# Performance work log

Measured on AMD Instinct MI355X. Metric: run time of the kernel, lower is better.

The kernel has to match this reference:

```python
import jax, jax.numpy as jnp
import numpy as np

NEG = -10000000000.0  # matches the torch module's additive mask value


def _span_attn(enc, logit_tok, starts, ends, qb, bsz):
    # enc: [bsz, seq, d]; logit_tok: [bsz, seq]; starts/ends/qb: [Q]
    seq = enc.shape[1]
    pos = jnp.arange(seq)
    # span mask: token t belongs to span iff start <= t <= end (inclusive)
    mask = (pos[None, :] >= starts[:, None]) & (pos[None, :] <= ends[:, None])  # [Q, seq]
    logits = logit_tok[qb] + (1.0 - mask.astype(enc.dtype)) * NEG               # [Q, seq]
    w = jax.nn.softmax(logits, axis=1)                                           # [Q, seq]
    # avoid materializing enc[qb] ([Q, seq, d]): contract against every batch row,
    # then select the right batch with a one-hot (p is tiny: [Q, bsz, d]).
    p = jnp.einsum('qs,bsd->qbd', w, enc)
    oh = jax.nn.one_hot(qb, bsz, dtype=enc.dtype)
    return jnp.einsum('qbd,qb->qd', p, oh)


def setup_inputs() -> dict:
    key = jax.random.key(0)
    ks = jax.random.split(key, 10)
    bsz, seq, hd, pd, Q = 8, 2048, 1024, 256, 8192
    enc = jax.random.normal(ks[0], (bsz, seq, hd), dtype=jnp.float32)
    proj_w = jax.random.normal(ks[1], (hd, pd), dtype=jnp.float32) * (1.0 / np.sqrt(hd))
    proj_b = jnp.zeros((pd,), dtype=jnp.float32)
    attn_w = jax.random.normal(ks[2], (pd,), dtype=jnp.float32) * (1.0 / np.sqrt(pd))
    attn_b = jnp.zeros((), dtype=jnp.float32)

    def make_spans(k):
        k1, k2, k3 = jax.random.split(k, 3)
        s = jax.random.randint(k1, (Q,), 0, seq)
        ln = jax.random.randint(k2, (Q,), 0, 32)
        e = jnp.minimum(s + ln, seq - 1)
        return s, e

    s1, e1 = make_spans(ks[3])
    s2, e2 = make_spans(ks[4])
    qb = jax.random.randint(ks[5], (Q,), 0, bsz)
    return {
        'flag': 0,
        'encoded_input': enc,
        'start_ids_1': s1,
        'end_ids_1': e1,
        'query_batch_idx': qb,
        'start_ids_2': s2,
        'end_ids_2': e2,
        'proj_w': proj_w,
        'proj_b': proj_b,
        'attn_w': attn_w,
        'attn_b': attn_b,
    }


def reference(flag, encoded_input, start_ids_1, end_ids_1, query_batch_idx,
              start_ids_2, end_ids_2, proj_w, proj_b, attn_w, attn_b):
    del flag  # unused in the original forward
    bsz = encoded_input.shape[0]
    enc = encoded_input @ proj_w + proj_b                 # use_proj=True path
    logit_tok = jnp.einsum('bsd,d->bs', enc, attn_w) + attn_b  # Linear(d,1)
    res1 = _span_attn(enc, logit_tok, start_ids_1, end_ids_1, query_batch_idx, bsz)
    res2 = _span_attn(enc, logit_tok, start_ids_2, end_ids_2, query_batch_idx, bsz)
    return (res1, res2)
```

## Files before the change

kernel.cpp:

```cpp
#include <hip/hip_runtime.h>

typedef __attribute__((ext_vector_type(8))) short bf16x8;
typedef __attribute__((ext_vector_type(4))) float f32x4;

#define LDK 40

__device__ __forceinline__ float bf2f(unsigned short u) {
    union { unsigned int i; float f; } v; v.i = ((unsigned int)u) << 16; return v.f;
}
__device__ __forceinline__ unsigned short f2bf(float f) {
    union { float f; unsigned int i; } v; v.f = f;
    unsigned int x = v.i;
    return (unsigned short)((x + 0x7FFFu + ((x >> 16) & 1u)) >> 16);
}

__global__ __launch_bounds__(256) void transpose_b_kernel(
    const float* __restrict__ B, unsigned short* __restrict__ Bt, int K, int N)
{
    __shared__ float tile[32][33];
    int kb = blockIdx.x % (K / 32);
    int nb = blockIdx.x / (K / 32);
    int k0 = kb * 32, n0 = nb * 32;
    int tx = threadIdx.x & 31, ty = threadIdx.x >> 5;
    #pragma unroll
    for (int i = 0; i < 4; ++i)
        tile[ty + 8 * i][tx] = B[(size_t)(k0 + ty + 8 * i) * N + n0 + tx];
    __syncthreads();
    #pragma unroll
    for (int i = 0; i < 4; ++i)
        Bt[(size_t)(n0 + ty + 8 * i) * K + k0 + tx] = f2bf(tile[tx][ty + 8 * i]);
}

__global__ __launch_bounds__(256, 4) void gemm_mfma_kernel(
    const float* __restrict__ A, const unsigned short* __restrict__ Bt,
    const float* __restrict__ bias, unsigned short* __restrict__ C,
    int M, int N, int K)
{
    __shared__ unsigned short Asl[2][64 * LDK];
    __shared__ unsigned short Bsl[2][64 * LDK];

    const int tid = threadIdx.x;
    const int bid = blockIdx.x;
    const int xcd = bid & 7;
    const int j   = bid >> 3;
    const int bn  = (j & 3) * 64;
    const int bm  = (xcd * 32 + (j >> 2)) * 64;

    const int lane = tid & 63;
    const int wave = tid >> 6;
    const int wr = (wave >> 1) * 32;
    const int wc = (wave & 1) * 32;

    const int srow = tid >> 2;
    const int sk   = (tid & 3) * 8;
    const float*          Aptr = A  + (size_t)(bm + srow) * K + sk;
    const unsigned short* Bptr = Bt + (size_t)(bn + srow) * K + sk;

    float4 areg[2];
    uint4  breg;

    f32x4 acc[2][2];
    #pragma unroll
    for (int m = 0; m < 2; ++m)
        #pragma unroll
        for (int n = 0; n < 2; ++n)
            acc[m][n] = (f32x4){0.f, 0.f, 0.f, 0.f};

    const int c15 = lane & 15;
    const int kg8 = (lane >> 4) * 8;

    #define LOAD_TILE(k0)                                                     \
        {                                                                     \
            areg[0] = *(const float4*)(Aptr + (k0));                          \
            areg[1] = *(const float4*)(Aptr + (k0) + 4);                      \
            breg    = *(const uint4*)(Bptr + (k0));                           \
        }

    #define STORE_TILE(buf)                                                   \
        {                                                                     \
            unsigned short tmp[8];                                            \
            const float* af = (const float*)areg;                             \
            _Pragma("unroll")                                                 \
            for (int i = 0; i < 8; ++i) tmp[i] = f2bf(af[i]);                 \
            *(bf16x8*)&Asl[buf][srow * LDK + sk] = *(bf16x8*)&tmp[0];         \
            *(uint4*)&Bsl[buf][srow * LDK + sk]  = breg;                      \
        }

    const int nk = K / 32;

    LOAD_TILE(0)
    STORE_TILE(0)
    __syncthreads();

    for (int t = 0; t < nk; ++t) {
        if (t + 1 < nk) LOAD_TILE((t + 1) * 32)

        const int buf = t & 1;
        bf16x8 af[2], bfr[2];
        #pragma unroll
        for (int m = 0; m < 2; ++m)
            af[m] = *(bf16x8*)&Asl[buf][(wr + m * 16 + c15) * LDK + kg8];
        #pragma unroll
        for (int n = 0; n < 2; ++n)
            bfr[n] = *(bf16x8*)&Bsl[buf][(wc + n * 16 + c15) * LDK + kg8];
        #pragma unroll
        for (int m = 0; m < 2; ++m)
            #pragma unroll
            for (int n = 0; n < 2; ++n)
                acc[m][n] = __builtin_amdgcn_mfma_f32_16x16x32_bf16(
                    af[m], bfr[n], acc[m][n], 0, 0, 0);

        if (t + 1 < nk) {
            STORE_TILE((t + 1) & 1)
            __syncthreads();
        }
    }

    const int col0 = bn + wc + c15;
    const int row0 = bm + wr + (lane >> 4) * 4;
    #pragma unroll
    for (int n = 0; n < 2; ++n) {
        float bv = bias[col0 + n * 16];
        #pragma unroll
        for (int m = 0; m < 2; ++m) {
            #pragma unroll
            for (int i = 0; i < 4; ++i) {
                C[(size_t)(row0 + m * 16 + i) * N + col0 + n * 16] =
                    f2bf(acc[m][n][i] + bv);
            }
        }
    }
    #undef LOAD_TILE
    #undef STORE_TILE
}

__global__ __launch_bounds__(256) void logit_kernel(
    const unsigned short* __restrict__ enc, const float* __restrict__ attn_w,
    float* __restrict__ logit, int rows)
{
    int gid = blockIdx.x * 256 + threadIdx.x;
    int row = gid >> 6, lane = gid & 63;
    if (row >= rows) return;
    ushort4 ev = *(const ushort4*)(enc + (size_t)row * 256 + lane * 4);
    float4  w  = ((const float4*)attn_w)[lane];
    float s = bf2f(ev.x) * w.x + bf2f(ev.y) * w.y +
              bf2f(ev.z) * w.z + bf2f(ev.w) * w.w;
    #pragma unroll
    for (int off = 32; off; off >>= 1) s += __shfl_down(s, off, 64);
    if (lane == 0) logit[row] = s;
}

__global__ __launch_bounds__(256) void span_kernel(
    const unsigned short* __restrict__ enc, const float* __restrict__ logit,
    const int* __restrict__ s1, const int* __restrict__ e1,
    const int* __restrict__ s2, const int* __restrict__ e2,
    const int* __restrict__ qb, float* __restrict__ out,
    int Q, int seq, int pd)
{
    int lane = threadIdx.x & 63;
    int q = blockIdx.x * 4 + (threadIdx.x >> 6);
    int r  = (q >= Q) ? 1 : 0;
    int qi = q - r * Q;
    int s = r ? s2[qi] : s1[qi];
    int e = r ? e2[qi] : e1[qi];
    int b = qb[qi];
    int len = e - s + 1;

    const float* lp = logit + (size_t)b * seq + s;
    float lg = (lane < len) ? lp[lane] : -3.4e38f;
    float m = lg;
    #pragma unroll
    for (int off = 32; off; off >>= 1) m = fmaxf(m, __shfl_xor(m, off, 64));
    float p = (lane < len) ? __expf(lg - m) : 0.0f;
    float sum = p;
    #pragma unroll
    for (int off = 32; off; off >>= 1) sum += __shfl_xor(sum, off, 64);
    float inv = 1.0f / sum;

    const unsigned short* ep = enc + ((size_t)b * seq + s) * pd + lane * 4;
    float ax = 0.f, ay = 0.f, az = 0.f, aw = 0.f;

    int t = 0;
    for (; t + 8 <= len; t += 8) {
        ushort4 ev[8];
        #pragma unroll
        for (int u = 0; u < 8; ++u)
            ev[u] = *(const ushort4*)(ep + (size_t)(t + u) * pd);
        #pragma unroll
        for (int u = 0; u < 8; ++u) {
            float wt = __shfl(p, t + u, 64);
            ax += wt * bf2f(ev[u].x);
            ay += wt * bf2f(ev[u].y);
            az += wt * bf2f(ev[u].z);
            aw += wt * bf2f(ev[u].w);
        }
    }
    for (; t < len; ++t) {
        float wt = __shfl(p, t, 64);
        ushort4 ev = *(const ushort4*)(ep + (size_t)t * pd);
        ax += wt * bf2f(ev.x);
        ay += wt * bf2f(ev.y);
        az += wt * bf2f(ev.z);
        aw += wt * bf2f(ev.w);
    }
    float4 res = {ax * inv, ay * inv, az * inv, aw * inv};
    *((float4*)(out + (size_t)q * pd) + lane) = res;
}

extern "C" void kernel_launch(void* const* d_in, const int* in_sizes, int n_in,
                              void* d_out, int out_size, void* d_ws, size_t ws_size,
                              hipStream_t stream) {
    const float* enc_in = (const float*)d_in[1];
    const int*   s1     = (const int*)d_in[2];
    const int*   e1     = (const int*)d_in[3];
    const int*   qb     = (const int*)d_in[4];
    const int*   s2     = (const int*)d_in[5];
    const int*   e2     = (const int*)d_in[6];
    const float* proj_w = (const float*)d_in[7];
    const float* proj_b = (const float*)d_in[8];
    const float* attn_w = (const float*)d_in[9];
    float* out = (float*)d_out;

    const int Q   = in_sizes[2];
    const int pd  = in_sizes[8];
    const int hd  = in_sizes[7] / pd;
    const int seq = 2048;
    const int M   = in_sizes[1] / hd;

    unsigned short* enc_bf = (unsigned short*)d_ws;
    float*          logit  = (float*)((char*)d_ws + (size_t)M * pd * 2);
    unsigned short* Btw    = (unsigned short*)((char*)d_ws +
                               (size_t)M * pd * 2 + (size_t)M * 4);

    transpose_b_kernel<<<(hd / 32) * (pd / 32), 256, 0, stream>>>(proj_w, Btw, hd, pd);
    gemm_mfma_kernel<<<(M / 64) * (pd / 64), 256, 0, stream>>>(
        enc_in, Btw, proj_b, enc_bf, M, pd, hd);
    logit_kernel<<<M / 4, 256, 0, stream>>>(enc_bf, attn_w, logit, M);
    span_kernel<<<2 * Q / 4, 256, 0, stream>>>(
        enc_bf, logit, s1, e1, s2, e2, qb, out, Q, seq, pd);
}
```

Measured before the change: 170.3 us.

## Fuse logit into GEMM epilogue, async LDS B loads, pipeline GEMM, widen span loads

The per-token logit reduction moves into the GEMM epilogue, using shuffles and atomicAdd onto a buffer zeroed by a memset, and the separate logit kernel is dropped. The GEMM now loads B straight into LDS with global_load_lds into an XOR-swizzled layout. It also prefetches A two tiles ahead with manual waitcnt/barrier control and raised MFMA priority. The span kernel issues 16 clamped loads per step instead of 8 plus a scalar tail. This removes a kernel launch and a re-read of the projected activations, but adds atomics and an extra memset launch. Logits are now computed from fp32 values rather than bf16-rounded ones, so they change slightly.

```diff
diff --git a/kernel.cpp b/kernel.cpp
--- a/kernel.cpp
+++ b/kernel.cpp
@@ -13,6 +13,16 @@
     unsigned int x = v.i;
     return (unsigned short)((x + 0x7FFFu + ((x >> 16) & 1u)) >> 16);
 }
+
+__device__ __forceinline__ void gload16(const void* g, void* l) {
+    __builtin_amdgcn_global_load_lds(
+        (const __attribute__((address_space(1))) unsigned int*)g,
+        (__attribute__((address_space(3))) unsigned int*)l, 16, 0, 0);
+}
+
+#define ASM_LGKM0 { asm volatile("s_waitcnt lgkmcnt(0)" ::: "memory"); \
+                    __builtin_amdgcn_sched_barrier(0); }
+#define ASM_BAR   asm volatile("s_barrier" ::: "memory")
 
 __global__ __launch_bounds__(256) void transpose_b_kernel(
     const float* __restrict__ B, unsigned short* __restrict__ Bt, int K, int N)
@@ -33,11 +43,12 @@
 
 __global__ __launch_bounds__(256, 4) void gemm_mfma_kernel(
     const float* __restrict__ A, const unsigned short* __restrict__ Bt,
-    const float* __restrict__ bias, unsigned short* __restrict__ C,
+    const float* __restrict__ bias, const float* __restrict__ attn_w,
+    unsigned short* __restrict__ C, float* __restrict__ logit,
     int M, int N, int K)
 {
-    __shared__ unsigned short Asl[2][64 * LDK];
-    __shared__ unsigned short Bsl[2][64 * LDK];
+    __shared__ __attribute__((aligned(16))) unsigned short AsA[2][64 * LDK];
+    __shared__ __attribute__((aligned(16))) unsigned short AsB[2][64 * 32];
 
     const int tid = threadIdx.x;
     const int bid = blockIdx.x;
@@ -53,12 +64,15 @@
 
     const int srow = tid >> 2;
     const int sk   = (tid & 3) * 8;
-    const float*          Aptr = A  + (size_t)(bm + srow) * K + sk;
-    const unsigned short* Bptr = Bt + (size_t)(bn + srow) * K + sk;
-
-    float4 areg[2];
-    uint4  breg;
-
+    const float* Aptr = A + (size_t)(bm + srow) * K + sk;
+
+    const int brow = 16 * wave + (lane >> 2);
+    const int bsl  = (lane & 3) ^ ((lane >> 3) & 3);
+    const unsigned short* Bptr = Bt + (size_t)(bn + brow) * K + bsl * 8;
+    unsigned short* ldsB0 = &AsB[0][wave * 512];
+    unsigned short* ldsB1 = &AsB[1][wave * 512];
+
+    float4 areg[2][2];
     f32x4 acc[2][2];
     #pragma unroll
     for (int m = 0; m < 2; ++m)
@@ -67,87 +81,96 @@
             acc[m][n] = (f32x4){0.f, 0.f, 0.f, 0.f};
 
     const int c15 = lane & 15;
-    const int kg8 = (lane >> 4) * 8;
-
-    #define LOAD_TILE(k0)                                                     \
-        {                                                                     \
-            areg[0] = *(const float4*)(Aptr + (k0));                          \
-            areg[1] = *(const float4*)(Aptr + (k0) + 4);                      \
-            breg    = *(const uint4*)(Bptr + (k0));                           \
-        }
-
-    #define STORE_TILE(buf)                                                   \
-        {                                                                     \
+    const int g4  = lane >> 4;
+    const int kg8 = g4 * 8;
+    const int slB = (g4 ^ ((c15 >> 1) & 3)) * 8;
+
+    const int nk = K / 32;
+
+    gload16(Bptr, ldsB0);
+    areg[0][0] = *(const float4*)(Aptr);
+    areg[0][1] = *(const float4*)(Aptr + 4);
+    asm volatile("s_waitcnt vmcnt(0)" ::: "memory");
+    {
+        unsigned short tmp[8];
+        const float* afp = (const float*)areg[0];
+        #pragma unroll
+        for (int i = 0; i < 8; ++i) tmp[i] = f2bf(afp[i]);
+        *(bf16x8*)&AsA[0][srow * LDK + sk] = *(bf16x8*)&tmp[0];
+    }
+    gload16(Bptr + 32, ldsB1);
+    areg[1][0] = *(const float4*)(Aptr + 32);
+    areg[1][1] = *(const float4*)(Aptr + 36);
+    ASM_LGKM0;
+    ASM_BAR;
+
+#define BODY(T, S)                                                            \
+    {                                                                         \
+        bf16x8 af0 = *(bf16x8*)&AsA[S][(wr + c15) * LDK + kg8];               \
+        bf16x8 af1 = *(bf16x8*)&AsA[S][(wr + 16 + c15) * LDK + kg8];          \
+        bf16x8 bf0 = *(bf16x8*)&AsB[S][(wc + c15) * 32 + slB];                \
+        bf16x8 bf1 = *(bf16x8*)&AsB[S][(wc + 16 + c15) * 32 + slB];           \
+        ASM_LGKM0;                                                            \
+        ASM_BAR;                            \
+        if ((T) + 2 < nk) {                                                   \
+            gload16(Bptr + ((T) + 2) * 32, (S) ? ldsB1 : ldsB0);              \
+            areg[S][0] = *(const float4*)(Aptr + ((T) + 2) * 32);             \
+            areg[S][1] = *(const float4*)(Aptr + ((T) + 2) * 32 + 4);         \
+        }                                                                     \
+        __builtin_amdgcn_s_setprio(1);                                        \
+        acc[0][0] = __builtin_amdgcn_mfma_f32_16x16x32_bf16(af0, bf0, acc[0][0], 0, 0, 0); \
+        acc[0][1] = __builtin_amdgcn_mfma_f32_16x16x32_bf16(af0, bf1, acc[0][1], 0, 0, 0); \
+        acc[1][0] = __builtin_amdgcn_mfma_f32_16x16x32_bf16(af1, bf0, acc[1][0], 0, 0, 0); \
+        acc[1][1] = __builtin_amdgcn_mfma_f32_16x16x32_bf16(af1, bf1, acc[1][1], 0, 0, 0); \
+        __builtin_amdgcn_s_setprio(0);                                        \
+        if ((T) + 1 < nk) {                                                   \
+            if ((T) + 2 < nk) { asm volatile("s_waitcnt vmcnt(3)" ::: "memory"); } \
+            else              { asm volatile("s_waitcnt vmcnt(0)" ::: "memory"); } \
             unsigned short tmp[8];                                            \
-            const float* af = (const float*)areg;                             \
+            const float* afp = (const float*)areg[1 - (S)];                   \
             _Pragma("unroll")                                                 \
-            for (int i = 0; i < 8; ++i) tmp[i] = f2bf(af[i]);                 \
-            *(bf16x8*)&Asl[buf][srow * LDK + sk] = *(bf16x8*)&tmp[0];         \
-            *(uint4*)&Bsl[buf][srow * LDK + sk]  = breg;                      \
-        }
-
-    const int nk = K / 32;
-
-    LOAD_TILE(0)
-    STORE_TILE(0)
-    __syncthreads();
-
-    for (int t = 0; t < nk; ++t) {
-        if (t + 1 < nk) LOAD_TILE((t + 1) * 32)
-
-        const int buf = t & 1;
-        bf16x8 af[2], bfr[2];
-        #pragma unroll
-        for (int m = 0; m < 2; ++m)
-            af[m] = *(bf16x8*)&Asl[buf][(wr + m * 16 + c15) * LDK + kg8];
-        #pragma unroll
-        for (int n = 0; n < 2; ++n)
-            bfr[n] = *(bf16x8*)&Bsl[buf][(wc + n * 16 + c15) * LDK + kg8];
-        #pragma unroll
-        for (int m = 0; m < 2; ++m)
-            #pragma unroll
-            for (int n = 0; n < 2; ++n)
-                acc[m][n] = __builtin_amdgcn_mfma_f32_16x16x32_bf16(
-                    af[m], bfr[n], acc[m][n], 0, 0, 0);
-
-        if (t + 1 < nk) {
-            STORE_TILE((t + 1) & 1)
-            __syncthreads();
-        }
-    }
+            for (int i = 0; i < 8; ++i) tmp[i] = f2bf(afp[i]);                \
+            *(bf16x8*)&AsA[1 - (S)][srow * LDK + sk] = *(bf16x8*)&tmp[0];     \
+            ASM_LGKM0;                                                        \
+        }                                                                     \
+        ASM_BAR;                                           \
+    }
+
+    for (int t = 0; t < nk; t += 2) {
+        BODY(t, 0)
+        BODY(t + 1, 1)
+    }
+#undef BODY
 
     const int col0 = bn + wc + c15;
-    const int row0 = bm + wr + (lane >> 4) * 4;
+    const int row0 = bm + wr + g4 * 4;
+    float wsum[2][4] = {};
     #pragma unroll
     for (int n = 0; n < 2; ++n) {
-        float bv = bias[col0 + n * 16];
+        float bv  = bias[col0 + n * 16];
+        float awv = attn_w[col0 + n * 16];
         #pragma unroll
         for (int m = 0; m < 2; ++m) {
             #pragma unroll
             for (int i = 0; i < 4; ++i) {
-                C[(size_t)(row0 + m * 16 + i) * N + col0 + n * 16] =
-                    f2bf(acc[m][n][i] + bv);
+                float cf = acc[m][n][i] + bv;
+                C[(size_t)(row0 + m * 16 + i) * N + col0 + n * 16] = f2bf(cf);
+                wsum[m][i] += cf * awv;
             }
         }
     }
-    #undef LOAD_TILE
-    #undef STORE_TILE
-}
-
-__global__ __launch_bounds__(256) void logit_kernel(
-    const unsigned short* __restrict__ enc, const float* __restrict__ attn_w,
-    float* __restrict__ logit, int rows)
-{
-    int gid = blockIdx.x * 256 + threadIdx.x;
-    int row = gid >> 6, lane = gid & 63;
-    if (row >= rows) return;
-    ushort4 ev = *(const ushort4*)(enc + (size_t)row * 256 + lane * 4);
-    float4  w  = ((const float4*)attn_w)[lane];
-    float s = bf2f(ev.x) * w.x + bf2f(ev.y) * w.y +
-              bf2f(ev.z) * w.z + bf2f(ev.w) * w.w;
-    #pragma unroll
-    for (int off = 32; off; off >>= 1) s += __shfl_down(s, off, 64);
-    if (lane == 0) logit[row] = s;
+    #pragma unroll
+    for (int m = 0; m < 2; ++m) {
+        #pragma unroll
+        for (int i = 0; i < 4; ++i) {
+            float v = wsum[m][i];
+            v += __shfl_xor(v, 1, 64);
+            v += __shfl_xor(v, 2, 64);
+            v += __shfl_xor(v, 4, 64);
+            v += __shfl_xor(v, 8, 64);
+            if (c15 == 0) atomicAdd(&logit[row0 + m * 16 + i], v);
+        }
+    }
 }
 
 __global__ __launch_bounds__(256) void span_kernel(
@@ -180,28 +203,22 @@
     const unsigned short* ep = enc + ((size_t)b * seq + s) * pd + lane * 4;
     float ax = 0.f, ay = 0.f, az = 0.f, aw = 0.f;
 
-    int t = 0;
-    for (; t + 8 <= len; t += 8) {
-        ushort4 ev[8];
-        #pragma unroll
-        for (int u = 0; u < 8; ++u)
-            ev[u] = *(const ushort4*)(ep + (size_t)(t + u) * pd);
-        #pragma unroll
-        for (int u = 0; u < 8; ++u) {
-            float wt = __shfl(p, t + u, 64);
+    for (int t0 = 0; t0 < len; t0 += 16) {
+        ushort4 ev[16];
+        #pragma unroll
+        for (int u = 0; u < 16; ++u) {
+            int tc = t0 + u;
+            tc = (tc < len) ? tc : (len - 1);
+            ev[u] = *(const ushort4*)(ep + (size_t)tc * pd);
+        }
+        #pragma unroll
+        for (int u = 0; u < 16; ++u) {
+            float wt = __shfl(p, t0 + u, 64);
             ax += wt * bf2f(ev[u].x);
             ay += wt * bf2f(ev[u].y);
             az += wt * bf2f(ev[u].z);
             aw += wt * bf2f(ev[u].w);
         }
-    }
-    for (; t < len; ++t) {
-        float wt = __shfl(p, t, 64);
-        ushort4 ev = *(const ushort4*)(ep + (size_t)t * pd);
-        ax += wt * bf2f(ev.x);
-        ay += wt * bf2f(ev.y);
-        az += wt * bf2f(ev.z);
-        aw += wt * bf2f(ev.w);
     }
     float4 res = {ax * inv, ay * inv, az * inv, aw * inv};
     *((float4*)(out + (size_t)q * pd) + lane) = res;
@@ -232,10 +249,10 @@
     unsigned short* Btw    = (unsigned short*)((char*)d_ws +
                                (size_t)M * pd * 2 + (size_t)M * 4);
 
+    hipMemsetAsync(logit, 0, (size_t)M * sizeof(float), stream);
     transpose_b_kernel<<<(hd / 32) * (pd / 32), 256, 0, stream>>>(proj_w, Btw, hd, pd);
     gemm_mfma_kernel<<<(M / 64) * (pd / 64), 256, 0, stream>>>(
-        enc_in, Btw, proj_b, enc_bf, M, pd, hd);
-    logit_kernel<<<M / 4, 256, 0, stream>>>(enc_bf, attn_w, logit, M);
+        enc_in, Btw, proj_b, attn_w, enc_bf, logit, M, pd, hd);
     span_kernel<<<2 * Q / 4, 256, 0, stream>>>(
         enc_bf, logit, s1, e1, s2, e2, qb, out, Q, seq, pd);
 }
```

Measured after the change: 172.7 us. About the same (+1.4%).
